# Kernel tuning notes

Measured on AMD Instinct MI355X. Metric: run time of the kernel, lower is better.

Reference implementation:

```python
import jax, jax.numpy as jnp
import numpy as np

N = 1_000_000  # nodes
E = 4_000_000  # edges (avg degree 4)
F_IN, F_HID, F_OUT = 18, 16, 2


def setup_inputs() -> dict:
    key = jax.random.key(0)
    ks = jax.random.split(key, 6)
    x = jax.random.normal(ks[0], (N, F_IN), dtype=jnp.float32)
    edge_index = jax.random.randint(ks[1], (2, E), 0, N, dtype=jnp.int32)
    # Glorot-ish init for the two GCNConv weight matrices + zero biases (PyG default)
    W1 = jax.random.normal(ks[2], (F_IN, F_HID), dtype=jnp.float32) * (1.0 / np.sqrt(F_IN))
    b1 = jnp.zeros((F_HID,), dtype=jnp.float32)
    W2 = jax.random.normal(ks[3], (F_HID, F_OUT), dtype=jnp.float32) * (1.0 / np.sqrt(F_HID))
    b2 = jnp.zeros((F_OUT,), dtype=jnp.float32)
    return {"x": x, "W1": W1, "b1": b1, "W2": W2, "b2": b2, "edge_index": edge_index}


def reference(x, W1, b1, W2, b2, edge_index):
    n = x.shape[0]
    # PyG GCNConv: add self-loops, symmetric normalization D^-1/2 A D^-1/2
    loops = jnp.arange(n, dtype=edge_index.dtype)
    row = jnp.concatenate([edge_index[0], loops])  # source
    col = jnp.concatenate([edge_index[1], loops])  # target
    ones = jnp.ones(row.shape[0], dtype=x.dtype)
    deg = jax.ops.segment_sum(ones, col, num_segments=n)
    dis = jnp.where(deg > 0, jax.lax.rsqrt(jnp.maximum(deg, 1.0)), 0.0)
    norm = dis[row] * dis[col]  # [E+N]

    def gcn_conv(h, W, b):
        hw = h @ W                               # [N, F] small dense GEMM
        msg = hw[row] * norm[:, None]            # gather + scale  [E+N, F]
        agg = jax.ops.segment_sum(msg, col, num_segments=n)  # scatter-add
        return agg + b

    h = jax.nn.relu(gcn_conv(x, W1, b1))
    # F.dropout(training=self.training) -> identity in eval mode
    out = gcn_conv(h, W2, b2)
    return jax.nn.log_softmax(out, axis=1)
```

## Files before the change

kernel.cpp:

```cpp
#include <hip/hip_runtime.h>

#define ABLK 512
#define PBLK 512
#define PITER 32
#define EPB (PBLK * PITER)
#define F_INK 18
#define F_HIDK 16
#define CB 2048
#define CSH 11
#define MAXNC 512
#define CAPB 10240
#define SCAP CAPB

__device__ __forceinline__ unsigned f2bf(float f) {
  unsigned u = __float_as_uint(f);
  return (u + 0x7fffu + ((u >> 16) & 1u)) >> 16;
}
__device__ __forceinline__ float bflo(unsigned u) { return __uint_as_float(u << 16); }
__device__ __forceinline__ float bfhi(unsigned u) { return __uint_as_float(u & 0xffff0000u); }

__global__ __launch_bounds__(PBLK) void k_pre(const int* __restrict__ rows,
                                              const int* __restrict__ cols,
                                              int* __restrict__ gcur,
                                              unsigned* __restrict__ epk,
                                              const float* __restrict__ x,
                                              const float* __restrict__ W1,
                                              uint4* __restrict__ hwb,
                                              int e, int n, int NC, int nblk) {
  __shared__ int hist[MAXNC];
  __shared__ int cur[MAXNC];
  __shared__ float xf[PBLK * F_INK];
  if (blockIdx.x < nblk) {
    for (int j = threadIdx.x; j < NC; j += PBLK) hist[j] = 0;
    __syncthreads();
    const int base = blockIdx.x * EPB;
    const int4* cols4 = (const int4*)(cols + base);
    const int4* rows4 = (const int4*)(rows + base);
    int4 c4[PITER / 4], r4[PITER / 4];
#pragma unroll
    for (int k = 0; k < PITER / 4; ++k) {
      int idx = k * PBLK + threadIdx.x;
      int gi = base + idx * 4;
      if (gi + 3 < e) {
        c4[k] = cols4[idx];
        r4[k] = rows4[idx];
      } else {
        int cc[4], rr[4];
        for (int j = 0; j < 4; ++j) {
          int g = gi + j;
          if (g < e) { cc[j] = cols[g]; rr[j] = rows[g]; }
          else       { cc[j] = -1; rr[j] = 0; }
        }
        c4[k] = make_int4(cc[0], cc[1], cc[2], cc[3]);
        r4[k] = make_int4(rr[0], rr[1], rr[2], rr[3]);
      }
      int cc[4] = {c4[k].x, c4[k].y, c4[k].z, c4[k].w};
#pragma unroll
      for (int j = 0; j < 4; ++j)
        if (cc[j] >= 0) atomicAdd(&hist[cc[j] >> CSH], 1);
    }
    __syncthreads();
    for (int b = threadIdx.x; b < NC; b += PBLK) {
      int c = hist[b];
      int off = (c > 0) ? atomicAdd(&gcur[b], c) : 0;
      cur[b] = b * CAPB + off;
    }
    __syncthreads();
#pragma unroll
    for (int k = 0; k < PITER / 4; ++k) {
      int cc[4] = {c4[k].x, c4[k].y, c4[k].z, c4[k].w};
      int rr[4] = {r4[k].x, r4[k].y, r4[k].z, r4[k].w};
#pragma unroll
      for (int j = 0; j < 4; ++j) {
        if (cc[j] >= 0) {
          int bb = cc[j] >> CSH;
          int p = atomicAdd(&cur[bb], 1);
          if (p < (bb + 1) * CAPB)
            epk[p] = ((unsigned)(cc[j] & (CB - 1)) << 20) | (unsigned)rr[j];
        }
      }
    }
  } else {
    const int hb = blockIdx.x - nblk;
#pragma unroll
    for (int g = 0; g < CB / PBLK; ++g) {
      const int gbase = hb * CB + g * PBLK;
      if (gbase >= n) break;
      const int nrow = min(PBLK, n - gbase);
      const int lim = nrow * F_INK;
      __syncthreads();
      for (int t = threadIdx.x; t < lim; t += PBLK)
        xf[t] = x[(size_t)gbase * F_INK + t];
      __syncthreads();
      if (threadIdx.x < (unsigned)nrow) {
        int node = gbase + (int)threadIdx.x;
        float hw[F_HIDK];
#pragma unroll
        for (int f = 0; f < F_HIDK; ++f) hw[f] = 0.0f;
        const float* xi = &xf[threadIdx.x * F_INK];
#pragma unroll
        for (int k = 0; k < F_INK; ++k) {
          float xk = xi[k];
#pragma unroll
          for (int f = 0; f < F_HIDK; ++f) hw[f] = fmaf(xk, W1[k * F_HIDK + f], hw[f]);
        }
        unsigned w[8];
#pragma unroll
        for (int p = 0; p < 8; ++p)
          w[p] = f2bf(hw[2 * p]) | (f2bf(hw[2 * p + 1]) << 16);
        hwb[(size_t)node * 2 + 0] = make_uint4(w[0], w[1], w[2], w[3]);
        hwb[(size_t)node * 2 + 1] = make_uint4(w[4], w[5], w[6], w[7]);
      }
    }
  }
}

__global__ __launch_bounds__(PBLK) void k_sortB(const unsigned* __restrict__ epk,
                                                const int* __restrict__ gcnt,
                                                const uint4* __restrict__ hwb,
                                                unsigned* __restrict__ sorted2,
                                                int2* __restrict__ noderng,
                                                float* __restrict__ dis,
                                                uint4* __restrict__ s1b, int n) {
  __shared__ int hist[CB];
  __shared__ int psum[PBLK];
  __shared__ unsigned stage[SCAP];
  const int b = blockIdx.x;
  const int s = b * CAPB;
  const int cnt = min(gcnt[b], CAPB);
  for (int j = threadIdx.x; j < CB; j += PBLK) hist[j] = 0;
  __syncthreads();
  const int cnt4 = cnt >> 2;
  const uint4* epk4 = (const uint4*)(epk + s);
  for (int i = threadIdx.x; i < cnt4; i += PBLK) {
    uint4 v = epk4[i];
    atomicAdd(&hist[v.x >> 20], 1);
    atomicAdd(&hist[v.y >> 20], 1);
    atomicAdd(&hist[v.z >> 20], 1);
    atomicAdd(&hist[v.w >> 20], 1);
  }
  for (int i = cnt4 * 4 + threadIdx.x; i < cnt; i += PBLK)
    atomicAdd(&hist[epk[s + i] >> 20], 1);
  __syncthreads();
  int loc[4];
  int sum = 0;
#pragma unroll
  for (int k = 0; k < 4; ++k) {
    int c = hist[threadIdx.x * 4 + k];
    loc[k] = sum;
    sum += c;
  }
  psum[threadIdx.x] = sum;
  __syncthreads();
  for (int off = 1; off < PBLK; off <<= 1) {
    int tv = (threadIdx.x >= off) ? psum[threadIdx.x - off] : 0;
    __syncthreads();
    psum[threadIdx.x] += tv;
    __syncthreads();
  }
  const int base0 = psum[threadIdx.x] - sum;
#pragma unroll
  for (int k = 0; k < 4; ++k) {
    int j = threadIdx.x * 4 + k;
    int bj = base0 + loc[k];
    int cj = ((k < 3) ? loc[k + 1] : sum) - loc[k];
    int node = (b << CSH) + j;
    if (node < n) {
      noderng[node] = make_int2(s + bj, s + bj + cj);
      dis[node] = rsqrtf((float)(cj + 1));
    }
    hist[j] = bj;
  }
  __syncthreads();
  for (int i = threadIdx.x; i < cnt; i += PBLK) {
    unsigned rec = epk[s + i];
    int p = atomicAdd(&hist[rec >> 20], 1);
    stage[p] = rec & 0xFFFFFu;
  }
  __syncthreads();
  uint4* so4 = (uint4*)(sorted2 + s);
  const uint4* st4 = (const uint4*)stage;
  for (int j = threadIdx.x; j < cnt4; j += PBLK) so4[j] = st4[j];
  for (int j = cnt4 * 4 + threadIdx.x; j < cnt; j += PBLK) sorted2[s + j] = stage[j];
#pragma unroll
  for (int g = 0; g < CB / PBLK; ++g) {
    int node = (b << CSH) + g * PBLK + (int)threadIdx.x;
    if (node < n) {
      float di = dis[node];
      uint4 a0 = hwb[(size_t)node * 2 + 0];
      uint4 a1 = hwb[(size_t)node * 2 + 1];
      unsigned w0 = f2bf(bflo(a0.x) * di) | (f2bf(bfhi(a0.x) * di) << 16);
      unsigned w1 = f2bf(bflo(a0.y) * di) | (f2bf(bfhi(a0.y) * di) << 16);
      unsigned w2 = f2bf(bflo(a0.z) * di) | (f2bf(bfhi(a0.z) * di) << 16);
      unsigned w3 = f2bf(bflo(a0.w) * di) | (f2bf(bfhi(a0.w) * di) << 16);
      unsigned w4 = f2bf(bflo(a1.x) * di) | (f2bf(bfhi(a1.x) * di) << 16);
      unsigned w5 = f2bf(bflo(a1.y) * di) | (f2bf(bfhi(a1.y) * di) << 16);
      unsigned w6 = f2bf(bflo(a1.z) * di) | (f2bf(bfhi(a1.z) * di) << 16);
      unsigned w7 = f2bf(bflo(a1.w) * di) | (f2bf(bfhi(a1.w) * di) << 16);
      s1b[(size_t)node * 2 + 0] = make_uint4(w0, w1, w2, w3);
      s1b[(size_t)node * 2 + 1] = make_uint4(w4, w5, w6, w7);
    }
  }
}

#define ACC8(V)                                         \
  acc[0] += bflo(V.x); acc[1] += bfhi(V.x);             \
  acc[2] += bflo(V.y); acc[3] += bfhi(V.y);             \
  acc[4] += bflo(V.z); acc[5] += bfhi(V.z);             \
  acc[6] += bflo(V.w); acc[7] += bfhi(V.w);

__global__ __launch_bounds__(ABLK) void k_agg1(const unsigned* __restrict__ sorted2,
                                               const int2* __restrict__ noderng,
                                               const uint4* __restrict__ s1b,
                                               const float* __restrict__ dis,
                                               const float* __restrict__ b1,
                                               const float* __restrict__ W2,
                                               unsigned* __restrict__ s2b, int n) {
  const int q = threadIdx.x & 1;
  const int node = blockIdx.x * (ABLK >> 1) + (threadIdx.x >> 1);
  if (node >= n) return;
  float di = dis[node];
  uint4 sv = s1b[(size_t)node * 2 + q];
  float acc[8] = {bflo(sv.x), bfhi(sv.x), bflo(sv.y), bfhi(sv.y),
                  bflo(sv.z), bfhi(sv.z), bflo(sv.w), bfhi(sv.w)};
  int2 rng = noderng[node];
  int i = rng.x;
  const int re = rng.y;
  const int len = re - i;
  if (len > 0) {
    uint4 v0 = s1b[(size_t)sorted2[i] * 2 + q];
    if (len > 1) {
      uint4 v1 = s1b[(size_t)sorted2[i + 1] * 2 + q];
      i += 2;
      while (i < re) {
        uint4 v2 = s1b[(size_t)sorted2[i] * 2 + q];
        ACC8(v0);
        v0 = v1; v1 = v2;
        ++i;
      }
      ACC8(v0);
      v0 = v1;
    }
    ACC8(v0);
  }
  float p0 = 0.f, p1 = 0.f;
#pragma unroll
  for (int k = 0; k < 8; ++k) {
    int f = q * 8 + k;
    float h = fmaxf(fmaf(di, acc[k], b1[f]), 0.0f);
    p0 = fmaf(h, W2[f * 2 + 0], p0);
    p1 = fmaf(h, W2[f * 2 + 1], p1);
  }
  p0 += __shfl_xor(p0, 1);
  p1 += __shfl_xor(p1, 1);
  if (q == 0)
    s2b[node] = f2bf(p0 * di) | (f2bf(p1 * di) << 16);
}

__global__ __launch_bounds__(ABLK) void k_agg2(const unsigned* __restrict__ sorted2,
                                               const int2* __restrict__ noderng,
                                               const unsigned* __restrict__ s2b,
                                               const float* __restrict__ dis,
                                               const float* __restrict__ b2,
                                               float* __restrict__ out, int n) {
  const int node = blockIdx.x * ABLK + threadIdx.x;
  if (node >= n) return;
  float di = dis[node];
  unsigned sv = s2b[node];
  float a0 = bflo(sv), a1 = bfhi(sv);
  int2 rng = noderng[node];
  int i = rng.x;
  const int re = rng.y;
  const int len = re - i;
  if (len > 0) {
    unsigned v0 = s2b[sorted2[i]];
    if (len > 1) {
      unsigned v1 = s2b[sorted2[i + 1]];
      i += 2;
      while (i < re) {
        unsigned v2 = s2b[sorted2[i]];
        a0 += bflo(v0); a1 += bfhi(v0);
        v0 = v1; v1 = v2;
        ++i;
      }
      a0 += bflo(v0); a1 += bfhi(v0);
      v0 = v1;
    }
    a0 += bflo(v0); a1 += bfhi(v0);
  }
  float o0 = fmaf(di, a0, b2[0]);
  float o1 = fmaf(di, a1, b2[1]);
  float m = fmaxf(o0, o1);
  float lse = m + logf(expf(o0 - m) + expf(o1 - m));
  float2 r;
  r.x = o0 - lse;
  r.y = o1 - lse;
  ((float2*)out)[node] = r;
}

extern "C" void kernel_launch(void* const* d_in, const int* in_sizes, int n_in,
                              void* d_out, int out_size, void* d_ws, size_t ws_size,
                              hipStream_t stream) {
  const float* x  = (const float*)d_in[0];
  const float* W1 = (const float*)d_in[1];
  const float* b1 = (const float*)d_in[2];
  const float* W2 = (const float*)d_in[3];
  const float* b2 = (const float*)d_in[4];
  const int*   ei = (const int*)d_in[5];
  const int n = in_sizes[0] / F_INK;
  const int e = in_sizes[5] / 2;
  const int* rows = ei;
  const int* cols = ei + e;

  const int NC = (n + CB - 1) / CB;
  const int nblk = (e + EPB - 1) / EPB;

  char* ws = (char*)d_ws;
  size_t off = 0;
  auto alloc = [&](size_t bytes) {
    void* p = ws + off;
    off = (off + bytes + 15) & ~(size_t)15;
    return p;
  };
  float* dis        = (float*)alloc((size_t)n * 4);
  uint4* hwb        = (uint4*)alloc((size_t)n * 32);
  uint4* s1b        = (uint4*)alloc((size_t)n * 32);
  unsigned* s2b     = (unsigned*)alloc((size_t)n * 4);
  unsigned* epk     = (unsigned*)alloc((size_t)NC * CAPB * 4);
  unsigned* sorted2 = (unsigned*)alloc((size_t)NC * CAPB * 4);
  int2* noderng     = (int2*)alloc((size_t)n * 8);
  int* gcur         = (int*)alloc((size_t)NC * 4);
  float* outp = (float*)d_out;

  (void)hipMemsetAsync(gcur, 0, (size_t)NC * 4, stream);
  k_pre  <<<nblk + NC, PBLK, 0, stream>>>(rows, cols, gcur, epk, x, W1, hwb,
                                          e, n, NC, nblk);
  k_sortB<<<NC, PBLK, 0, stream>>>(epk, gcur, hwb, sorted2, noderng, dis, s1b, n);
  k_agg1 <<<(n + (ABLK / 2) - 1) / (ABLK / 2), ABLK, 0, stream>>>(sorted2, noderng, s1b,
                                                                  dis, b1, W2, s2b, n);
  k_agg2 <<<(n + ABLK - 1) / ABLK, ABLK, 0, stream>>>(sorted2, noderng, s2b, dis, b2,
                                                      outp, n);
}
```

Before: 183.6 us.

## Stage bucketed edges in shared memory before coalesced global writes

```diff
diff --git a/kernel.cpp b/kernel.cpp
--- a/kernel.cpp
+++ b/kernel.cpp
@@ -2,7 +2,7 @@
 
 #define ABLK 512
 #define PBLK 512
-#define PITER 32
+#define PITER 16
 #define EPB (PBLK * PITER)
 #define F_INK 18
 #define F_HIDK 16
@@ -11,6 +11,7 @@
 #define MAXNC 512
 #define CAPB 10240
 #define SCAP CAPB
+#define PSTG (PBLK * F_INK)
 
 __device__ __forceinline__ unsigned f2bf(float f) {
   unsigned u = __float_as_uint(f);
@@ -28,18 +29,21 @@
                                               uint4* __restrict__ hwb,
                                               int e, int n, int NC, int nblk) {
   __shared__ int hist[MAXNC];
-  __shared__ int cur[MAXNC];
-  __shared__ float xf[PBLK * F_INK];
+  __shared__ int lb[MAXNC];
+  __shared__ int gb[MAXNC];
+  __shared__ unsigned stage[PSTG];
+  const int tid = threadIdx.x;
   if (blockIdx.x < nblk) {
-    for (int j = threadIdx.x; j < NC; j += PBLK) hist[j] = 0;
+    for (int j = tid; j < NC; j += PBLK) hist[j] = 0;
     __syncthreads();
     const int base = blockIdx.x * EPB;
+    const int cnt = min(EPB, e - base);
     const int4* cols4 = (const int4*)(cols + base);
     const int4* rows4 = (const int4*)(rows + base);
     int4 c4[PITER / 4], r4[PITER / 4];
 #pragma unroll
     for (int k = 0; k < PITER / 4; ++k) {
-      int idx = k * PBLK + threadIdx.x;
+      int idx = k * PBLK + tid;
       int gi = base + idx * 4;
       if (gi + 3 < e) {
         c4[k] = cols4[idx];
@@ -60,10 +64,19 @@
         if (cc[j] >= 0) atomicAdd(&hist[cc[j] >> CSH], 1);
     }
     __syncthreads();
-    for (int b = threadIdx.x; b < NC; b += PBLK) {
-      int c = hist[b];
-      int off = (c > 0) ? atomicAdd(&gcur[b], c) : 0;
-      cur[b] = b * CAPB + off;
+    int v = (tid < NC) ? hist[tid] : 0;
+    lb[tid] = v;
+    __syncthreads();
+    for (int off = 1; off < MAXNC; off <<= 1) {
+      int tv = (tid >= off) ? lb[tid - off] : 0;
+      __syncthreads();
+      lb[tid] += tv;
+      __syncthreads();
+    }
+    lb[tid] -= v;
+    if (tid < NC) {
+      gb[tid] = (v > 0) ? atomicAdd(&gcur[tid], v) + tid * CAPB : 0;
+      hist[tid] = lb[tid];
     }
     __syncthreads();
 #pragma unroll
@@ -74,13 +87,23 @@
       for (int j = 0; j < 4; ++j) {
         if (cc[j] >= 0) {
           int bb = cc[j] >> CSH;
-          int p = atomicAdd(&cur[bb], 1);
-          if (p < (bb + 1) * CAPB)
-            epk[p] = ((unsigned)(cc[j] & (CB - 1)) << 20) | (unsigned)rr[j];
+          int p = atomicAdd(&hist[bb], 1);
+          stage[p] = ((unsigned)(cc[j] & (CB - 1)) << 20) | (unsigned)rr[j];
         }
       }
     }
+    __syncthreads();
+    for (int j = tid; j < cnt; j += PBLK) {
+      int lo = 0, hi = NC - 1;
+      while (lo < hi) {
+        int mid = (lo + hi + 1) >> 1;
+        if (lb[mid] <= j) lo = mid; else hi = mid - 1;
+      }
+      int dest = gb[lo] + (j - lb[lo]);
+      if (dest < (lo + 1) * CAPB) epk[dest] = stage[j];
+    }
   } else {
+    float* xf = (float*)stage;
     const int hb = blockIdx.x - nblk;
 #pragma unroll
     for (int g = 0; g < CB / PBLK; ++g) {
@@ -89,15 +112,15 @@
       const int nrow = min(PBLK, n - gbase);
       const int lim = nrow * F_INK;
       __syncthreads();
-      for (int t = threadIdx.x; t < lim; t += PBLK)
+      for (int t = tid; t < lim; t += PBLK)
         xf[t] = x[(size_t)gbase * F_INK + t];
       __syncthreads();
-      if (threadIdx.x < (unsigned)nrow) {
-        int node = gbase + (int)threadIdx.x;
+      if (tid < nrow) {
+        int node = gbase + tid;
         float hw[F_HIDK];
 #pragma unroll
         for (int f = 0; f < F_HIDK; ++f) hw[f] = 0.0f;
-        const float* xi = &xf[threadIdx.x * F_INK];
+        const float* xi = &xf[tid * F_INK];
 #pragma unroll
         for (int k = 0; k < F_INK; ++k) {
           float xk = xi[k];
```

Result: no change. 185.7 us (+1.1%).
